# Optimization experiments

Hardware: AMD Instinct MI355X
Metric: run time of the kernel (lower is better)

## Reference

```python
import jax, jax.numpy as jnp
import numpy as np

N = 100000   # nodes
E = 1600000  # edges (avg degree 16)
D = 64       # feature dim (in_dim)


def setup_inputs() -> dict:
    key = jax.random.key(0)
    k1, k2, k3, k4, k5 = jax.random.split(key, 5)
    h = jax.random.normal(k1, (N, D), dtype=jnp.float32)
    dnorm = jax.random.uniform(k2, (N,), dtype=jnp.float32)  # deg^-1/2 proxy
    # xavier_normal_(gain=1.414) for Linear(2D, 1): std = gain*sqrt(2/(fan_in+fan_out))
    std = 1.414 * np.sqrt(2.0 / (2 * D + 1))
    gate_w = jax.random.normal(k3, (1, 2 * D), dtype=jnp.float32) * std
    gate_b = jnp.zeros((1,), dtype=jnp.float32)
    src = jax.random.randint(k4, (E,), 0, N, dtype=jnp.int32)
    dst = jax.random.randint(k5, (E,), 0, N, dtype=jnp.int32)
    return {"h": h, "dnorm": dnorm, "gate_w": gate_w, "gate_b": gate_b,
            "src": src, "dst": dst}


def reference(h, dnorm, gate_w, gate_b, src, dst):
    # gate(cat[h_dst, h_src]) == h_dst @ W[:, :D].T + h_src @ W[:, D:].T + b
    w_dst = gate_w[0, :D]  # [D]
    w_src = gate_w[0, D:]  # [D]
    h_src = h[src]                                        # [E, D] gather
    g = jnp.tanh(h[dst] @ w_dst + h_src @ w_src + gate_b[0])  # [E]
    e = g * dnorm[dst] * dnorm[src]                       # [E] (dropout p=0 -> identity)
    # u_mul_e + sum: z[v] = sum_{(u->v)} h[u] * e
    z = jax.ops.segment_sum(h_src * e[:, None], dst, num_segments=N)  # [N, D]
    return z
```

## Files before the change

### kernel.cpp

```cpp
#include <hip/hip_runtime.h>
#include <hip/hip_bf16.h>

#define D 64
#define BKT_SHIFT 7
#define BKT_NODES 128
#define NB_CNT 1024
#define DSPLIT_T 1024
#define DSPLIT_E 2048
#define CAP 2560
#define QBINS 512

__device__ __forceinline__ unsigned short f2bf(float x) {
    unsigned u = __float_as_uint(x);
    unsigned r = 0x7fffu + ((u >> 16) & 1u);
    return (unsigned short)((u + r) >> 16);
}

template<bool MAKE_BF16>
__global__ void fal_precompute(const float* __restrict__ h,
                               const float* __restrict__ dnorm,
                               const float* __restrict__ gate_w,
                               const float* __restrict__ gate_b,
                               float2* __restrict__ sd,
                               float2* __restrict__ ss,
                               unsigned short* __restrict__ hb,
                               int* __restrict__ bcursor,
                               int nb, int N) {
    int tid  = threadIdx.x;
    if (blockIdx.x == 0) {
        for (int i = tid; i < nb; i += 256) bcursor[i] = 0;
    }
    int lane = tid & 63;
    int wave = tid >> 6;
    int grp  = lane >> 4;
    int gl   = lane & 15;

    int node = blockIdx.x * 16 + wave * 4 + grp;
    int nc   = node < N ? node : N - 1;

    const float4* h4 = (const float4*)h;
    const float4* w4 = (const float4*)gate_w;

    float4 hv  = h4[nc * 16 + gl];
    float4 wd  = w4[gl];
    float4 wsr = w4[16 + gl];

    if (MAKE_BF16 && node < N) {
        ushort4 p = make_ushort4(f2bf(hv.x), f2bf(hv.y), f2bf(hv.z), f2bf(hv.w));
        *(ushort4*)&hb[(size_t)node * D + gl * 4] = p;
    }

    float a = hv.x * wd.x + hv.y * wd.y + hv.z * wd.z + hv.w * wd.w;
    float b = hv.x * wsr.x + hv.y * wsr.y + hv.z * wsr.z + hv.w * wsr.w;

    for (int off = 1; off < 16; off <<= 1) {
        a += __shfl_xor(a, off, 64);
        b += __shfl_xor(b, off, 64);
    }

    if (gl == 0 && node < N) {
        float dn = dnorm[node];
        sd[node] = make_float2(a + gate_b[0], dn);
        ss[node] = make_float2(b, dn);
    }
}

__global__ __launch_bounds__(DSPLIT_T) void fal_multisplit(
        const int* __restrict__ src,
        const int* __restrict__ dst,
        int* __restrict__ bcursor,
        unsigned* __restrict__ pk_bin,
        int E, int nb) {
    __shared__ int lcount[NB_CNT];
    __shared__ int lscan[NB_CNT];
    __shared__ int gofs[NB_CNT];
    __shared__ int wsum16[16];
    __shared__ unsigned s_pk[DSPLIT_E];
    __shared__ int s_gpos[DSPLIT_E];

    int tid  = threadIdx.x;
    int lane = tid & 63;
    int w    = tid >> 6;
    lcount[tid] = 0;
    __syncthreads();

    int E2 = E >> 1;
    int i2 = blockIdx.x * DSPLIT_T + tid;

    int srcs[2], dsts[2], lr[2];
    bool act = (i2 < E2);
    if (act) {
        int2 s2 = ((const int2*)src)[i2];
        int2 d2 = ((const int2*)dst)[i2];
        srcs[0] = s2.x; srcs[1] = s2.y;
        dsts[0] = d2.x; dsts[1] = d2.y;
        #pragma unroll
        for (int j = 0; j < 2; ++j)
            lr[j] = atomicAdd(&lcount[dsts[j] >> BKT_SHIFT], 1);
    }
    __syncthreads();

    int v = lcount[tid];
    for (int off = 1; off < 64; off <<= 1) {
        int t = __shfl_up(v, off, 64);
        if (lane >= off) v += t;
    }
    if (lane == 63) wsum16[w] = v;
    __syncthreads();
    if (tid < 16) {
        int s = wsum16[tid];
        for (int off = 1; off < 16; off <<= 1) {
            int t = __shfl_up(s, off, 64);
            if (tid >= off) s += t;
        }
        wsum16[tid] = s;
    }
    __syncthreads();
    lscan[tid] = v + (w ? wsum16[w - 1] : 0);

    if (tid < nb) {
        int c = lcount[tid];
        int rel = c ? atomicAdd(&bcursor[tid], c) : 0;
        gofs[tid] = tid * CAP + rel;
    }
    __syncthreads();

    if (act) {
        #pragma unroll
        for (int j = 0; j < 2; ++j) {
            int b = dsts[j] >> BKT_SHIFT;
            int lpos = (lscan[b] - lcount[b]) + lr[j];
            unsigned dl = (unsigned)(dsts[j] & (BKT_NODES - 1));
            s_pk[lpos] = (dl << 20) | (unsigned)srcs[j];
            int gp = gofs[b] + lr[j];
            s_gpos[lpos] = (gp < (b + 1) * CAP) ? gp : -1;
        }
    }
    __syncthreads();

    int total = lscan[NB_CNT - 1];
    for (int t = tid; t < total; t += DSPLIT_T) {
        int g = s_gpos[t];
        if (g >= 0) pk_bin[g] = s_pk[t];
    }
}

#define DRAIN(SEG0, DG, A0, A1, A2, A3, A4, A5, A6, A7) do {             \
    int k_ = 0;                                                          \
    for (; k_ + 2 <= (DG); k_ += 2) {                                    \
        int s0_ = (int)(s_srt[(SEG0) + k_]     & 0xFFFFFu);              \
        int s1_ = (int)(s_srt[(SEG0) + k_ + 1] & 0xFFFFFu);              \
        float e0_ = s_esc[(SEG0) + k_];                                  \
        float e1_ = s_esc[(SEG0) + k_ + 1];                              \
        if constexpr (BF16) {                                            \
            uint4 r0_ = *(const uint4*)&hb[(size_t)s0_ * D + cbase];     \
            uint4 r1_ = *(const uint4*)&hb[(size_t)s1_ * D + cbase];     \
            A0 = fmaf(__uint_as_float(r0_.x << 16),         e0_, A0);    \
            A1 = fmaf(__uint_as_float(r0_.x & 0xffff0000u), e0_, A1);    \
            A2 = fmaf(__uint_as_float(r0_.y << 16),         e0_, A2);    \
            A3 = fmaf(__uint_as_float(r0_.y & 0xffff0000u), e0_, A3);    \
            A4 = fmaf(__uint_as_float(r0_.z << 16),         e0_, A4);    \
            A5 = fmaf(__uint_as_float(r0_.z & 0xffff0000u), e0_, A5);    \
            A6 = fmaf(__uint_as_float(r0_.w << 16),         e0_, A6);    \
            A7 = fmaf(__uint_as_float(r0_.w & 0xffff0000u), e0_, A7);    \
            A0 = fmaf(__uint_as_float(r1_.x << 16),         e1_, A0);    \
            A1 = fmaf(__uint_as_float(r1_.x & 0xffff0000u), e1_, A1);    \
            A2 = fmaf(__uint_as_float(r1_.y << 16),         e1_, A2);    \
            A3 = fmaf(__uint_as_float(r1_.y & 0xffff0000u), e1_, A3);    \
            A4 = fmaf(__uint_as_float(r1_.z << 16),         e1_, A4);    \
            A5 = fmaf(__uint_as_float(r1_.z & 0xffff0000u), e1_, A5);    \
            A6 = fmaf(__uint_as_float(r1_.w << 16),         e1_, A6);    \
            A7 = fmaf(__uint_as_float(r1_.w & 0xffff0000u), e1_, A7);    \
        } else {                                                         \
            const float4* hp0_ = (const float4*)&h[(size_t)s0_ * D + cbase]; \
            const float4* hp1_ = (const float4*)&h[(size_t)s1_ * D + cbase]; \
            float4 q0_ = hp0_[0], q1_ = hp0_[1], q2_ = hp1_[0], q3_ = hp1_[1]; \
            A0 = fmaf(q0_.x, e0_, A0); A1 = fmaf(q0_.y, e0_, A1);        \
            A2 = fmaf(q0_.z, e0_, A2); A3 = fmaf(q0_.w, e0_, A3);        \
            A4 = fmaf(q1_.x, e0_, A4); A5 = fmaf(q1_.y, e0_, A5);        \
            A6 = fmaf(q1_.z, e0_, A6); A7 = fmaf(q1_.w, e0_, A7);        \
            A0 = fmaf(q2_.x, e1_, A0); A1 = fmaf(q2_.y, e1_, A1);        \
            A2 = fmaf(q2_.z, e1_, A2); A3 = fmaf(q2_.w, e1_, A3);        \
            A4 = fmaf(q3_.x, e1_, A4); A5 = fmaf(q3_.y, e1_, A5);        \
            A6 = fmaf(q3_.z, e1_, A6); A7 = fmaf(q3_.w, e1_, A7);        \
        }                                                                \
    }                                                                    \
    if (k_ < (DG)) {                                                     \
        int s0_ = (int)(s_srt[(SEG0) + k_] & 0xFFFFFu);                  \
        float e0_ = s_esc[(SEG0) + k_];                                  \
        if constexpr (BF16) {                                            \
            uint4 r0_ = *(const uint4*)&hb[(size_t)s0_ * D + cbase];     \
            A0 = fmaf(__uint_as_float(r0_.x << 16),         e0_, A0);    \
            A1 = fmaf(__uint_as_float(r0_.x & 0xffff0000u), e0_, A1);    \
            A2 = fmaf(__uint_as_float(r0_.y << 16),         e0_, A2);    \
            A3 = fmaf(__uint_as_float(r0_.y & 0xffff0000u), e0_, A3);    \
            A4 = fmaf(__uint_as_float(r0_.z << 16),         e0_, A4);    \
            A5 = fmaf(__uint_as_float(r0_.z & 0xffff0000u), e0_, A5);    \
            A6 = fmaf(__uint_as_float(r0_.w << 16),         e0_, A6);    \
            A7 = fmaf(__uint_as_float(r0_.w & 0xffff0000u), e0_, A7);    \
        } else {                                                         \
            const float4* hp0_ = (const float4*)&h[(size_t)s0_ * D + cbase]; \
            float4 q0_ = hp0_[0], q1_ = hp0_[1];                         \
            A0 = fmaf(q0_.x, e0_, A0); A1 = fmaf(q0_.y, e0_, A1);        \
            A2 = fmaf(q0_.z, e0_, A2); A3 = fmaf(q0_.w, e0_, A3);        \
            A4 = fmaf(q1_.x, e0_, A4); A5 = fmaf(q1_.y, e0_, A5);        \
            A6 = fmaf(q1_.z, e0_, A6); A7 = fmaf(q1_.w, e0_, A7);        \
        }                                                                \
    }                                                                    \
} while (0)

template<bool BF16>
__global__ __launch_bounds__(512) void fal_bucket_process(
        const float* __restrict__ h,
        const unsigned short* __restrict__ hb,
        const float2* __restrict__ sd,
        const float2* __restrict__ ss,
        const int* __restrict__ bcursor,
        const unsigned* __restrict__ pk_bin,
        float* __restrict__ z, int N) {
    __shared__ unsigned s_pk[CAP];
    __shared__ unsigned s_srt[CAP];
    __shared__ float    s_esc[CAP];
    __shared__ float2   sdl[BKT_NODES];
    __shared__ int qhist[QBINS];
    __shared__ int qbase[QBINS];
    __shared__ int qcur[QBINS];
    __shared__ int wsum8[8];

    int b    = blockIdx.x;
    int tid  = threadIdx.x;
    int lane = tid & 63;
    int w    = tid >> 6;

    qhist[tid] = 0;
    if (tid < BKT_NODES) {
        int node = b * BKT_NODES + tid;
        sdl[tid] = (node < N) ? sd[node] : make_float2(0.f, 0.f);
    }
    __syncthreads();

    int cnt = min(bcursor[b], CAP);
    const unsigned* bin = pk_bin + (size_t)b * CAP;

    for (int t = tid; t < cnt; t += 512) {
        unsigned pk = bin[t];
        s_pk[t] = pk;
        int key = (int)(((pk & 0xFFFFFu) >> 15) * 128u + (pk >> 20));
        atomicAdd(&qhist[key], 1);
    }
    __syncthreads();

    int myh = qhist[tid];
    int v = myh;
    for (int off = 1; off < 64; off <<= 1) {
        int t = __shfl_up(v, off, 64);
        if (lane >= off) v += t;
    }
    if (lane == 63) wsum8[w] = v;
    __syncthreads();
    if (tid < 8) {
        int s2 = wsum8[tid];
        for (int off = 1; off < 8; off <<= 1) {
            int t = __shfl_up(s2, off, 64);
            if (tid >= off) s2 += t;
        }
        wsum8[tid] = s2;
    }
    __syncthreads();
    {
        int incl = v + (w ? wsum8[w - 1] : 0);
        qbase[tid] = incl - myh;
        qcur[tid]  = 0;
    }
    __syncthreads();

    for (int t = tid; t < cnt; t += 512) {
        unsigned pk = s_pk[t];
        int dl = (int)(pk >> 20);
        int sn = (int)(pk & 0xFFFFFu);
        int key = (sn >> 15) * 128 + dl;
        int r  = atomicAdd(&qcur[key], 1);
        float2 sv = ss[sn];
        float2 dv = sdl[dl];
        float esc = tanhf(dv.x + sv.x) * dv.y * sv.y;
        int p = qbase[key] + r;
        s_srt[p] = pk;
        s_esc[p] = esc;
    }
    __syncthreads();

    int oct   = tid >> 3;
    int sdim  = tid & 7;
    int cbase = sdim * 8;

    float a0 = 0.f, a1 = 0.f, a2 = 0.f, a3 = 0.f;
    float a4 = 0.f, a5 = 0.f, a6 = 0.f, a7 = 0.f;
    float b0 = 0.f, b1 = 0.f, b2 = 0.f, b3 = 0.f;
    float b4 = 0.f, b5 = 0.f, b6 = 0.f, b7 = 0.f;

    for (int q = 0; q < 4; ++q) {
        int keyA = q * 128 + oct;
        int segA = qbase[keyA];
        int dgA  = qhist[keyA];
        DRAIN(segA, dgA, a0, a1, a2, a3, a4, a5, a6, a7);

        int keyB = q * 128 + oct + 64;
        int segB = qbase[keyB];
        int dgB  = qhist[keyB];
        DRAIN(segB, dgB, b0, b1, b2, b3, b4, b5, b6, b7);

        __syncthreads();
    }

    int nodeA = b * BKT_NODES + oct;
    if (nodeA < N) {
        float4* zp = (float4*)&z[(size_t)nodeA * D + cbase];
        zp[0] = make_float4(a0, a1, a2, a3);
        zp[1] = make_float4(a4, a5, a6, a7);
    }
    int nodeB = b * BKT_NODES + oct + 64;
    if (nodeB < N) {
        float4* zp = (float4*)&z[(size_t)nodeB * D + cbase];
        zp[0] = make_float4(b0, b1, b2, b3);
        zp[1] = make_float4(b4, b5, b6, b7);
    }
}

extern "C" void kernel_launch(void* const* d_in, const int* in_sizes, int n_in,
                              void* d_out, int out_size, void* d_ws, size_t ws_size,
                              hipStream_t stream) {
    const float* h      = (const float*)d_in[0];
    const float* dnorm  = (const float*)d_in[1];
    const float* gate_w = (const float*)d_in[2];
    const float* gate_b = (const float*)d_in[3];
    const int*   src    = (const int*)d_in[4];
    const int*   dst    = (const int*)d_in[5];
    float*       z      = (float*)d_out;

    int N  = in_sizes[1];
    int E  = in_sizes[4];
    int nb = (N + BKT_NODES - 1) >> BKT_SHIFT;

    char* ws0 = (char*)d_ws;
    size_t off = 0;
    auto alloc = [&](size_t bytes) {
        char* p = ws0 + off;
        off += (bytes + 15) & ~(size_t)15;
        return p;
    };
    float2*   sd      = (float2*)alloc((size_t)N * sizeof(float2));
    float2*   ss      = (float2*)alloc((size_t)N * sizeof(float2));
    int*      bcursor = (int*)alloc((size_t)nb * sizeof(int));
    unsigned* pk_bin  = (unsigned*)alloc((size_t)nb * CAP * sizeof(unsigned));
    unsigned short* hb = (unsigned short*)(ws0 + off);
    size_t need_with_hb = off + (size_t)N * D * sizeof(unsigned short);
    bool use_bf16 = (ws_size >= need_with_hb);

    if (use_bf16)
        fal_precompute<true><<<(N + 15) / 16, 256, 0, stream>>>(
            h, dnorm, gate_w, gate_b, sd, ss, hb, bcursor, nb, N);
    else
        fal_precompute<false><<<(N + 15) / 16, 256, 0, stream>>>(
            h, dnorm, gate_w, gate_b, sd, ss, hb, bcursor, nb, N);

    fal_multisplit<<<(E + DSPLIT_E - 1) / DSPLIT_E, DSPLIT_T, 0, stream>>>(
        src, dst, bcursor, pk_bin, E, nb);

    if (use_bf16)
        fal_bucket_process<true><<<nb, 512, 0, stream>>>(
            h, hb, sd, ss, bcursor, pk_bin, z, N);
    else
        fal_bucket_process<false><<<nb, 512, 0, stream>>>(
            h, hb, sd, ss, bcursor, pk_bin, z, N);
}
```

Before: 160.0 us.

## Split each bucket across four 128-thread blocks by destination slice

The bucket-processing kernel now launches four 128-thread blocks per 128-node bucket. Each block filters the bucket's packed edges down to its own 32-node destination slice, sorts them by source range and destination, and accumulates only those nodes. This raises the block count and cuts shared memory per block, aiming for better occupancy and load spread. The cost is that every block re-reads the whole bucket from global memory twice, and edges beyond a 768-entry cap are silently dropped. Separately, the multisplit kernel now handles four edges per thread using int4 loads.

```diff
diff --git a/kernel.cpp b/kernel.cpp
--- a/kernel.cpp
+++ b/kernel.cpp
@@ -6,9 +6,11 @@
 #define BKT_NODES 128
 #define NB_CNT 1024
 #define DSPLIT_T 1024
-#define DSPLIT_E 2048
+#define DSPLIT_E 4096
 #define CAP 2560
-#define QBINS 512
+#define SLICE_NODES 32
+#define QB 128
+#define SRT_CAP 768
 
 __device__ __forceinline__ unsigned short f2bf(float x) {
     unsigned u = __float_as_uint(x);
@@ -84,18 +86,18 @@
     lcount[tid] = 0;
     __syncthreads();
 
-    int E2 = E >> 1;
-    int i2 = blockIdx.x * DSPLIT_T + tid;
-
-    int srcs[2], dsts[2], lr[2];
-    bool act = (i2 < E2);
+    int E4 = E >> 2;
+    int i4 = blockIdx.x * DSPLIT_T + tid;
+
+    int srcs[4], dsts[4], lr[4];
+    bool act = (i4 < E4);
     if (act) {
-        int2 s2 = ((const int2*)src)[i2];
-        int2 d2 = ((const int2*)dst)[i2];
-        srcs[0] = s2.x; srcs[1] = s2.y;
-        dsts[0] = d2.x; dsts[1] = d2.y;
+        int4 s4 = ((const int4*)src)[i4];
+        int4 d4 = ((const int4*)dst)[i4];
+        srcs[0] = s4.x; srcs[1] = s4.y; srcs[2] = s4.z; srcs[3] = s4.w;
+        dsts[0] = d4.x; dsts[1] = d4.y; dsts[2] = d4.z; dsts[3] = d4.w;
         #pragma unroll
-        for (int j = 0; j < 2; ++j)
+        for (int j = 0; j < 4; ++j)
             lr[j] = atomicAdd(&lcount[dsts[j] >> BKT_SHIFT], 1);
     }
     __syncthreads();
@@ -127,7 +129,7 @@
 
     if (act) {
         #pragma unroll
-        for (int j = 0; j < 2; ++j) {
+        for (int j = 0; j < 4; ++j) {
             int b = dsts[j] >> BKT_SHIFT;
             int lpos = (lscan[b] - lcount[b]) + lr[j];
             unsigned dl = (unsigned)(dsts[j] & (BKT_NODES - 1));
@@ -210,7 +212,7 @@
 } while (0)
 
 template<bool BF16>
-__global__ __launch_bounds__(512) void fal_bucket_process(
+__global__ __launch_bounds__(128) void fal_bucket_process(
         const float* __restrict__ h,
         const unsigned short* __restrict__ hb,
         const float2* __restrict__ sd,
@@ -218,35 +220,39 @@
         const int* __restrict__ bcursor,
         const unsigned* __restrict__ pk_bin,
         float* __restrict__ z, int N) {
-    __shared__ unsigned s_pk[CAP];
-    __shared__ unsigned s_srt[CAP];
-    __shared__ float    s_esc[CAP];
-    __shared__ float2   sdl[BKT_NODES];
-    __shared__ int qhist[QBINS];
-    __shared__ int qbase[QBINS];
-    __shared__ int qcur[QBINS];
-    __shared__ int wsum8[8];
-
-    int b    = blockIdx.x;
+    __shared__ unsigned s_srt[SRT_CAP];
+    __shared__ float    s_esc[SRT_CAP];
+    __shared__ float2   sdl[SLICE_NODES];
+    __shared__ int qhist[QB];
+    __shared__ int qbase[QB];
+    __shared__ int qcur[QB];
+    __shared__ int wsum2[2];
+
+    int bid  = blockIdx.x;
+    int b0   = bid >> 2;
+    int qb   = bid & 3;
+    int dlo  = qb * SLICE_NODES;
     int tid  = threadIdx.x;
     int lane = tid & 63;
     int w    = tid >> 6;
 
-    qhist[tid] = 0;
-    if (tid < BKT_NODES) {
-        int node = b * BKT_NODES + tid;
+    if (tid < QB) qhist[tid] = 0;
+    if (tid < SLICE_NODES) {
+        int node = b0 * BKT_NODES + dlo + tid;
         sdl[tid] = (node < N) ? sd[node] : make_float2(0.f, 0.f);
     }
     __syncthreads();
 
-    int cnt = min(bcursor[b], CAP);
-    const unsigned* bin = pk_bin + (size_t)b * CAP;
-
-    for (int t = tid; t < cnt; t += 512) {
+    int cnt = min(bcursor[b0], CAP);
+    const unsigned* bin = pk_bin + (size_t)b0 * CAP;
+
+    for (int t = tid; t < cnt; t += 128) {
         unsigned pk = bin[t];
-        s_pk[t] = pk;
-        int key = (int)(((pk & 0xFFFFFu) >> 15) * 128u + (pk >> 20));
-        atomicAdd(&qhist[key], 1);
+        int dl = (int)(pk >> 20);
+        if ((dl >> 5) == qb) {
+            int key = (int)((pk & 0xFFFFFu) >> 15) * SLICE_NODES + (dl & 31);
+            atomicAdd(&qhist[key], 1);
+        }
     }
     __syncthreads();
 
@@ -256,36 +262,30 @@
         int t = __shfl_up(v, off, 64);
         if (lane >= off) v += t;
     }
-    if (lane == 63) wsum8[w] = v;
-    __syncthreads();
-    if (tid < 8) {
-        int s2 = wsum8[tid];
-        for (int off = 1; off < 8; off <<= 1) {
-            int t = __shfl_up(s2, off, 64);
-            if (tid >= off) s2 += t;
-        }
-        wsum8[tid] = s2;
-    }
+    if (lane == 63) wsum2[w] = v;
     __syncthreads();
     {
-        int incl = v + (w ? wsum8[w - 1] : 0);
+        int incl = v + (w ? wsum2[0] : 0);
         qbase[tid] = incl - myh;
         qcur[tid]  = 0;
     }
     __syncthreads();
 
-    for (int t = tid; t < cnt; t += 512) {
-        unsigned pk = s_pk[t];
+    for (int t = tid; t < cnt; t += 128) {
+        unsigned pk = bin[t];
         int dl = (int)(pk >> 20);
+        if ((dl >> 5) != qb) continue;
         int sn = (int)(pk & 0xFFFFFu);
-        int key = (sn >> 15) * 128 + dl;
+        int key = (sn >> 15) * SLICE_NODES + (dl & 31);
         int r  = atomicAdd(&qcur[key], 1);
         float2 sv = ss[sn];
-        float2 dv = sdl[dl];
+        float2 dv = sdl[dl & 31];
         float esc = tanhf(dv.x + sv.x) * dv.y * sv.y;
         int p = qbase[key] + r;
-        s_srt[p] = pk;
-        s_esc[p] = esc;
+        if (p < SRT_CAP) {
+            s_srt[p] = pk;
+            s_esc[p] = esc;
+        }
     }
     __syncthreads();
 
@@ -295,34 +295,34 @@
 
     float a0 = 0.f, a1 = 0.f, a2 = 0.f, a3 = 0.f;
     float a4 = 0.f, a5 = 0.f, a6 = 0.f, a7 = 0.f;
-    float b0 = 0.f, b1 = 0.f, b2 = 0.f, b3 = 0.f;
-    float b4 = 0.f, b5 = 0.f, b6 = 0.f, b7 = 0.f;
+    float b0r = 0.f, b1r = 0.f, b2r = 0.f, b3r = 0.f;
+    float b4r = 0.f, b5r = 0.f, b6r = 0.f, b7r = 0.f;
 
     for (int q = 0; q < 4; ++q) {
-        int keyA = q * 128 + oct;
+        int keyA = q * SLICE_NODES + oct;
         int segA = qbase[keyA];
-        int dgA  = qhist[keyA];
+        int dgA  = min(qhist[keyA], max(0, SRT_CAP - segA));
         DRAIN(segA, dgA, a0, a1, a2, a3, a4, a5, a6, a7);
 
-        int keyB = q * 128 + oct + 64;
+        int keyB = q * SLICE_NODES + oct + 16;
         int segB = qbase[keyB];
-        int dgB  = qhist[keyB];
-        DRAIN(segB, dgB, b0, b1, b2, b3, b4, b5, b6, b7);
+        int dgB  = min(qhist[keyB], max(0, SRT_CAP - segB));
+        DRAIN(segB, dgB, b0r, b1r, b2r, b3r, b4r, b5r, b6r, b7r);
 
         __syncthreads();
     }
 
-    int nodeA = b * BKT_NODES + oct;
+    int nodeA = b0 * BKT_NODES + dlo + oct;
     if (nodeA < N) {
         float4* zp = (float4*)&z[(size_t)nodeA * D + cbase];
         zp[0] = make_float4(a0, a1, a2, a3);
         zp[1] = make_float4(a4, a5, a6, a7);
     }
-    int nodeB = b * BKT_NODES + oct + 64;
+    int nodeB = b0 * BKT_NODES + dlo + oct + 16;
     if (nodeB < N) {
         float4* zp = (float4*)&z[(size_t)nodeB * D + cbase];
-        zp[0] = make_float4(b0, b1, b2, b3);
-        zp[1] = make_float4(b4, b5, b6, b7);
+        zp[0] = make_float4(b0r, b1r, b2r, b3r);
+        zp[1] = make_float4(b4r, b5r, b6r, b7r);
     }
 }
 
@@ -367,9 +367,9 @@
         src, dst, bcursor, pk_bin, E, nb);
 
     if (use_bf16)
-        fal_bucket_process<true><<<nb, 512, 0, stream>>>(
+        fal_bucket_process<true><<<nb * 4, 128, 0, stream>>>(
             h, hb, sd, ss, bcursor, pk_bin, z, N);
     else
-        fal_bucket_process<false><<<nb, 512, 0, stream>>>(
+        fal_bucket_process<false><<<nb * 4, 128, 0, stream>>>(
             h, hb, sd, ss, bcursor, pk_bin, z, N);
 }
```

New measurement: 157.5 us. About the same (-1.6%).

## Split tail buckets across two blocks and widen multisplit to four edges per thread

Applied to the files above, without the earlier changes.

The multisplit kernel now loads four edges per thread with int4 vector loads, halving the number of blocks and the per-block scan/atomic overhead. The bucket-process grid is restructured so the buckets beyond a multiple of 256 (the partial last wave on 256 CUs) are each handled by two blocks covering 64 nodes each, to reduce tail-wave imbalance. Half blocks still redo the full bucket load, histogram and sort, so that work is duplicated. More shared-memory contention per multisplit block and E not divisible by 4 would drop tail edges.

```diff
diff --git a/kernel.cpp b/kernel.cpp
--- a/kernel.cpp
+++ b/kernel.cpp
@@ -6,7 +6,7 @@
 #define BKT_NODES 128
 #define NB_CNT 1024
 #define DSPLIT_T 1024
-#define DSPLIT_E 2048
+#define DSPLIT_E 4096
 #define CAP 2560
 #define QBINS 512
 
@@ -84,18 +84,18 @@
     lcount[tid] = 0;
     __syncthreads();
 
-    int E2 = E >> 1;
-    int i2 = blockIdx.x * DSPLIT_T + tid;
-
-    int srcs[2], dsts[2], lr[2];
-    bool act = (i2 < E2);
+    int E4 = E >> 2;
+    int i4 = blockIdx.x * DSPLIT_T + tid;
+
+    int srcs[4], dsts[4], lr[4];
+    bool act = (i4 < E4);
     if (act) {
-        int2 s2 = ((const int2*)src)[i2];
-        int2 d2 = ((const int2*)dst)[i2];
-        srcs[0] = s2.x; srcs[1] = s2.y;
-        dsts[0] = d2.x; dsts[1] = d2.y;
+        int4 s4 = ((const int4*)src)[i4];
+        int4 d4 = ((const int4*)dst)[i4];
+        srcs[0] = s4.x; srcs[1] = s4.y; srcs[2] = s4.z; srcs[3] = s4.w;
+        dsts[0] = d4.x; dsts[1] = d4.y; dsts[2] = d4.z; dsts[3] = d4.w;
         #pragma unroll
-        for (int j = 0; j < 2; ++j)
+        for (int j = 0; j < 4; ++j)
             lr[j] = atomicAdd(&lcount[dsts[j] >> BKT_SHIFT], 1);
     }
     __syncthreads();
@@ -127,7 +127,7 @@
 
     if (act) {
         #pragma unroll
-        for (int j = 0; j < 2; ++j) {
+        for (int j = 0; j < 4; ++j) {
             int b = dsts[j] >> BKT_SHIFT;
             int lpos = (lscan[b] - lcount[b]) + lr[j];
             unsigned dl = (unsigned)(dsts[j] & (BKT_NODES - 1));
@@ -217,7 +217,7 @@
         const float2* __restrict__ ss,
         const int* __restrict__ bcursor,
         const unsigned* __restrict__ pk_bin,
-        float* __restrict__ z, int N) {
+        float* __restrict__ z, int nfull, int N) {
     __shared__ unsigned s_pk[CAP];
     __shared__ unsigned s_srt[CAP];
     __shared__ float    s_esc[CAP];
@@ -227,10 +227,19 @@
     __shared__ int qcur[QBINS];
     __shared__ int wsum8[8];
 
-    int b    = blockIdx.x;
+    int bid  = blockIdx.x;
     int tid  = threadIdx.x;
     int lane = tid & 63;
     int w    = tid >> 6;
+
+    int b, h0, is_half;
+    if (bid < nfull) { b = bid; h0 = 0; is_half = 0; }
+    else {
+        int idx = bid - nfull;
+        b  = nfull + (idx >> 1);
+        h0 = (idx & 1) * 64;
+        is_half = 1;
+    }
 
     qhist[tid] = 0;
     if (tid < BKT_NODES) {
@@ -298,31 +307,38 @@
     float b0 = 0.f, b1 = 0.f, b2 = 0.f, b3 = 0.f;
     float b4 = 0.f, b5 = 0.f, b6 = 0.f, b7 = 0.f;
 
-    for (int q = 0; q < 4; ++q) {
-        int keyA = q * 128 + oct;
-        int segA = qbase[keyA];
-        int dgA  = qhist[keyA];
-        DRAIN(segA, dgA, a0, a1, a2, a3, a4, a5, a6, a7);
-
-        int keyB = q * 128 + oct + 64;
-        int segB = qbase[keyB];
-        int dgB  = qhist[keyB];
-        DRAIN(segB, dgB, b0, b1, b2, b3, b4, b5, b6, b7);
-
-        __syncthreads();
-    }
-
-    int nodeA = b * BKT_NODES + oct;
-    if (nodeA < N) {
-        float4* zp = (float4*)&z[(size_t)nodeA * D + cbase];
-        zp[0] = make_float4(a0, a1, a2, a3);
-        zp[1] = make_float4(a4, a5, a6, a7);
-    }
-    int nodeB = b * BKT_NODES + oct + 64;
-    if (nodeB < N) {
-        float4* zp = (float4*)&z[(size_t)nodeB * D + cbase];
-        zp[0] = make_float4(b0, b1, b2, b3);
-        zp[1] = make_float4(b4, b5, b6, b7);
+    if (!is_half) {
+        for (int q = 0; q < 4; ++q) {
+            int keyA = q * 128 + oct;
+            DRAIN(qbase[keyA], qhist[keyA], a0, a1, a2, a3, a4, a5, a6, a7);
+            int keyB = q * 128 + oct + 64;
+            DRAIN(qbase[keyB], qhist[keyB], b0, b1, b2, b3, b4, b5, b6, b7);
+            __syncthreads();
+        }
+        int nodeA = b * BKT_NODES + oct;
+        if (nodeA < N) {
+            float4* zp = (float4*)&z[(size_t)nodeA * D + cbase];
+            zp[0] = make_float4(a0, a1, a2, a3);
+            zp[1] = make_float4(a4, a5, a6, a7);
+        }
+        int nodeB = b * BKT_NODES + oct + 64;
+        if (nodeB < N) {
+            float4* zp = (float4*)&z[(size_t)nodeB * D + cbase];
+            zp[0] = make_float4(b0, b1, b2, b3);
+            zp[1] = make_float4(b4, b5, b6, b7);
+        }
+    } else {
+        for (int q = 0; q < 4; ++q) {
+            int keyA = q * 128 + h0 + oct;
+            DRAIN(qbase[keyA], qhist[keyA], a0, a1, a2, a3, a4, a5, a6, a7);
+            __syncthreads();
+        }
+        int nodeA = b * BKT_NODES + h0 + oct;
+        if (nodeA < N) {
+            float4* zp = (float4*)&z[(size_t)nodeA * D + cbase];
+            zp[0] = make_float4(a0, a1, a2, a3);
+            zp[1] = make_float4(a4, a5, a6, a7);
+        }
     }
 }
 
@@ -356,6 +372,9 @@
     size_t need_with_hb = off + (size_t)N * D * sizeof(unsigned short);
     bool use_bf16 = (ws_size >= need_with_hb);
 
+    int nfull = nb & ~255;
+    int grid3 = nfull + 2 * (nb - nfull);
+
     if (use_bf16)
         fal_precompute<true><<<(N + 15) / 16, 256, 0, stream>>>(
             h, dnorm, gate_w, gate_b, sd, ss, hb, bcursor, nb, N);
@@ -367,9 +386,9 @@
         src, dst, bcursor, pk_bin, E, nb);
 
     if (use_bf16)
-        fal_bucket_process<true><<<nb, 512, 0, stream>>>(
-            h, hb, sd, ss, bcursor, pk_bin, z, N);
+        fal_bucket_process<true><<<grid3, 512, 0, stream>>>(
+            h, hb, sd, ss, bcursor, pk_bin, z, nfull, N);
     else
-        fal_bucket_process<false><<<nb, 512, 0, stream>>>(
-            h, hb, sd, ss, bcursor, pk_bin, z, N);
-}
+        fal_bucket_process<false><<<grid3, 512, 0, stream>>>(
+            h, hb, sd, ss, bcursor, pk_bin, z, nfull, N);
+}
```

New measurement: 150.3 us. -6.1%, faster.
